# Kernel tuning notes

Hardware: AMD Instinct MI355X
Metric: run time of the kernel (lower is better)

## Reference

```python
import math
import jax, jax.numpy as jnp
from jax import lax
import numpy as np

N = 512          # transform size; frame size = 2N
B = 16           # batch
T = 2048         # number of frames; signal length = N*T
PI = math.pi


def _make_mdct_filter(n: int, normalize: bool = True) -> jnp.ndarray:
    # filter[k, 0, t] = cos(pi/N * (t + 0.5 + N/2) * (k + 0.5)) / sqrt(N)
    k = jnp.arange(n, dtype=jnp.float32).reshape(n, 1, 1)
    t = jnp.arange(2 * n, dtype=jnp.float32).reshape(1, 1, 2 * n)
    f = jnp.cos(PI / n * (t + 0.5 + n / 2) * (k + 0.5))
    if normalize:
        f = f / jnp.sqrt(jnp.float32(n))
    return f  # [N, 1, 2N]


def setup_inputs() -> dict:
    key = jax.random.key(0)
    x = jax.random.normal(key, (B, 1, N * T), dtype=jnp.float32)
    mdct_filter = _make_mdct_filter(N, normalize=True)
    return {"x": x, "mdct_filter": mdct_filter}


def reference(x, mdct_filter):
    # Equivalent of F.conv1d(x, filter, stride=N, padding=N)
    n = mdct_filter.shape[0]
    # x: [B, 1, N*T] -> out: [B, N, T+1]
    out = lax.conv_general_dilated(
        x, mdct_filter,
        window_strides=(n,),
        padding=[(n, n)],
        dimension_numbers=("NCH", "OIH", "NCH"),
    )
    return out
```

## Files before the change

kernel.cpp:

```cpp
#include <hip/hip_runtime.h>
#include <hip/hip_bf16.h>
#include <stdint.h>
#include <stddef.h>


constexpr int N_ = 512;
constexpr int T_ = 2048;
constexpr int B_ = 16;
constexpr int LEN = N_ * T_;
constexpr int FRAMES = T_ + 1;
constexpr int COLS = B_ * FRAMES;
constexpr int NT_TILES = 257;
constexpr int COLS_PAD = NT_TILES * 128;
constexpr int KF = 512;
constexpr int BK = 64;

typedef __attribute__((ext_vector_type(8))) _Float16 f16x8;
typedef __attribute__((ext_vector_type(4))) _Float16 f16x4;
typedef __attribute__((ext_vector_type(4))) float f32x4;

#define GLD16(gptr, lptr)                                                     \
  __builtin_amdgcn_global_load_lds(                                           \
      (const __attribute__((address_space(1))) unsigned int*)(gptr),          \
      (__attribute__((address_space(3))) unsigned int*)(lptr), 16, 0, 0)

__global__ void prep_filter(const float* __restrict__ f,
                            _Float16* __restrict__ D) {
  int idx = (blockIdx.x * 256 + threadIdx.x) * 4;
  int k = idx >> 9;
  int j = idx & 511;
  int t = (j < 256) ? j : (j + 256);
  const float4 v = *(const float4*)&f[k * 1024 + t];
  f16x4 h = {(_Float16)v.x, (_Float16)v.y, (_Float16)v.z, (_Float16)v.w};
  *(f16x4*)&D[k * KF + j] = h;
}

__global__ void fold_x(const float* __restrict__ x, _Float16* __restrict__ V) {
  const int blk = (blockIdx.x & 7) * 1028 + (blockIdx.x >> 3);
  const int c = blk * 4 + (threadIdx.x >> 6);
  const int l = threadIdx.x & 63;
  const bool mi = (l < 32);
  const int j0 = mi ? (l * 8) : (256 + (l - 32) * 8);
  const float sgn = mi ? -1.0f : 1.0f;
  float4 a0 = {0.f, 0.f, 0.f, 0.f}, a1 = {0.f, 0.f, 0.f, 0.f};
  float4 r0 = {0.f, 0.f, 0.f, 0.f}, r1 = {0.f, 0.f, 0.f, 0.f};
  if (c < COLS) {
    int b = (int)((unsigned)c / (unsigned)FRAMES);
    int o = c - b * FRAMES;
    const int lo = b * LEN;
    const int g = lo + o * N_ - N_;
    const int fb = g + (mi ? j0 : (j0 + 256));
    const int rb = g + (mi ? (504 - j0) : (1272 - j0));
    if ((unsigned)(fb - lo) <= (unsigned)(LEN - 8)) {
      a0 = *(const float4*)(x + fb);
      a1 = *(const float4*)(x + fb + 4);
    }
    if ((unsigned)(rb - lo) <= (unsigned)(LEN - 8)) {
      r0 = *(const float4*)(x + rb);
      r1 = *(const float4*)(x + rb + 4);
    }
  }
  f16x8 h;
  h[0] = (_Float16)__builtin_fmaf(sgn, r1.w, a0.x);
  h[1] = (_Float16)__builtin_fmaf(sgn, r1.z, a0.y);
  h[2] = (_Float16)__builtin_fmaf(sgn, r1.y, a0.z);
  h[3] = (_Float16)__builtin_fmaf(sgn, r1.x, a0.w);
  h[4] = (_Float16)__builtin_fmaf(sgn, r0.w, a1.x);
  h[5] = (_Float16)__builtin_fmaf(sgn, r0.z, a1.y);
  h[6] = (_Float16)__builtin_fmaf(sgn, r0.y, a1.z);
  h[7] = (_Float16)__builtin_fmaf(sgn, r0.x, a1.w);
  if (c < COLS_PAD) *(f16x8*)&V[(size_t)c * KF + j0] = h;
}

__global__ __launch_bounds__(256, 4) void gemm_fold(
    const _Float16* __restrict__ D, const _Float16* __restrict__ V,
    float* __restrict__ out) {
  __shared__ __align__(16) _Float16 As[128 * BK];
  __shared__ __align__(16) _Float16 Bs[128 * BK];

  const int id = blockIdx.x;
  const int xcd = id & 7;
  const int sb = id >> 3;
  const int nt = (sb >> 2) * 8 + xcd;
  if (nt >= NT_TILES) return;
  const int m0 = (sb & 3) * 128;
  const int n0 = nt * 128;

  const int tid = threadIdx.x;
  const int wid = tid >> 6;
  const int lane = tid & 63;
  const int quad = lane >> 4;
  const int l16 = lane & 15;
  const int mw = (wid >> 1) * 64;
  const int nw = (wid & 1) * 64;

  f32x4 acc[4][4];
#pragma unroll
  for (int i = 0; i < 4; ++i)
#pragma unroll
    for (int j = 0; j < 4; ++j) acc[i][j] = (f32x4){0.f, 0.f, 0.f, 0.f};

  for (int kt = 0; kt < KF / BK; ++kt) {
    const int kb = kt * BK;
    __syncthreads();
#pragma unroll
    for (int it = 0; it < 4; ++it) {
      const int S = it * 256 + tid;
      const int r = S >> 3;
      const int c = (S & 7) ^ (r & 7);
      const int goff = kb + c * 8;
      GLD16(D + (size_t)(m0 + r) * KF + goff, &As[S * 8]);
      GLD16(V + (size_t)(n0 + r) * KF + goff, &Bs[S * 8]);
    }
    __syncthreads();

#pragma unroll
    for (int ko = 0; ko < 2; ++ko) {
      f16x8 af[4], bf[4];
#pragma unroll
      for (int i = 0; i < 4; ++i) {
        int ra = mw + i * 16 + l16;
        int rb = nw + i * 16 + l16;
        int ca = ko * 4 + quad;
        af[i] = *(const f16x8*)&As[(ra * 8 + (ca ^ (ra & 7))) * 8];
        bf[i] = *(const f16x8*)&Bs[(rb * 8 + (ca ^ (rb & 7))) * 8];
      }
#pragma unroll
      for (int i = 0; i < 4; ++i)
#pragma unroll
        for (int j = 0; j < 4; ++j)
          acc[i][j] = __builtin_amdgcn_mfma_f32_16x16x32_f16(af[i], bf[j], acc[i][j], 0, 0, 0);
    }
  }

#pragma unroll
  for (int i = 0; i < 4; ++i) {
#pragma unroll
    for (int j = 0; j < 4; ++j) {
      int col = n0 + nw + j * 16 + l16;
      if (col < COLS) {
        int b = col / FRAMES;
        int o = col - b * FRAMES;
        int rowb = m0 + mw + i * 16 + quad * 4;
        float* op = out + (size_t)b * N_ * FRAMES + (size_t)rowb * FRAMES + o;
#pragma unroll
        for (int r = 0; r < 4; ++r) op[(size_t)r * FRAMES] = acc[i][j][r];
      }
    }
  }
}

__global__ void naive_conv(const float* __restrict__ x, const float* __restrict__ f,
                           float* __restrict__ out) {
  int col = blockIdx.x;
  int k = threadIdx.x;
  __shared__ float win[1024];
  int b = col / FRAMES;
  int o = col - b * FRAMES;
  const float* xb = x + (size_t)b * LEN;
  int g = o * N_ - N_;
  for (int t = threadIdx.x; t < 1024; t += 512) {
    int i = g + t;
    win[t] = (i >= 0 && i < LEN) ? xb[i] : 0.0f;
  }
  __syncthreads();
  float s = 0.0f;
  const float* fk = f + (size_t)k * 1024;
  for (int t = 0; t < 1024; ++t) s += win[t] * fk[t];
  out[(size_t)b * N_ * FRAMES + (size_t)k * FRAMES + o] = s;
}

extern "C" void kernel_launch(void* const* d_in, const int* in_sizes, int n_in,
                              void* d_out, int out_size, void* d_ws, size_t ws_size,
                              hipStream_t stream) {
  const float* x = (const float*)d_in[0];
  const float* f = (const float*)d_in[1];
  float* out = (float*)d_out;

  const size_t elems_D = (size_t)512 * 512;
  const size_t elems_V = (size_t)COLS_PAD * KF;
  const size_t need = (elems_D + elems_V) * sizeof(_Float16);

  if (ws_size < need) {
    naive_conv<<<COLS, 512, 0, stream>>>(x, f, out);
    return;
  }

  _Float16* D = (_Float16*)d_ws;
  _Float16* V = D + elems_D;

  prep_filter<<<256, 256, 0, stream>>>(f, D);
  fold_x<<<COLS_PAD / 4, 256, 0, stream>>>(x, V);
  gemm_fold<<<1056, 256, 0, stream>>>(D, V, out);
}
```

Before: 147.8 us.

## Double-buffer LDS tiles in the folded MDCT GEMM to overlap loads with MFMA

Splits the GEMM's shared-memory tiles into two ping-pong buffers. The loop is unrolled so the next K-slice's global-to-LDS loads are issued before computing on the current slice. This halves the barriers per K-step and hides load latency behind MFMA work. In exchange, LDS use per block doubles and the occupancy hint drops from 4 to 2 blocks per CU. Correctness also relies on the barrier waiting for the outstanding LDS DMA loads, which is only waited on explicitly for the first stage.

```diff
diff --git a/kernel.cpp b/kernel.cpp
--- a/kernel.cpp
+++ b/kernel.cpp
@@ -14,6 +14,7 @@
 constexpr int COLS_PAD = NT_TILES * 128;
 constexpr int KF = 512;
 constexpr int BK = 64;
+constexpr int TILE_H = 128 * BK;
 
 typedef __attribute__((ext_vector_type(8))) _Float16 f16x8;
 typedef __attribute__((ext_vector_type(4))) _Float16 f16x4;
@@ -72,11 +73,13 @@
   if (c < COLS_PAD) *(f16x8*)&V[(size_t)c * KF + j0] = h;
 }
 
-__global__ __launch_bounds__(256, 4) void gemm_fold(
+__global__ __launch_bounds__(256, 2) void gemm_fold(
     const _Float16* __restrict__ D, const _Float16* __restrict__ V,
     float* __restrict__ out) {
-  __shared__ __align__(16) _Float16 As[128 * BK];
-  __shared__ __align__(16) _Float16 Bs[128 * BK];
+  __shared__ __align__(16) _Float16 As0[TILE_H];
+  __shared__ __align__(16) _Float16 Bs0[TILE_H];
+  __shared__ __align__(16) _Float16 As1[TILE_H];
+  __shared__ __align__(16) _Float16 Bs1[TILE_H];
 
   const int id = blockIdx.x;
   const int xcd = id & 7;
@@ -100,38 +103,62 @@
 #pragma unroll
     for (int j = 0; j < 4; ++j) acc[i][j] = (f32x4){0.f, 0.f, 0.f, 0.f};
 
-  for (int kt = 0; kt < KF / BK; ++kt) {
-    const int kb = kt * BK;
+#define STAGE(AS, BS, KT)                                                     \
+  do {                                                                        \
+    const int kb_ = (KT) * BK;                                                \
+    _Pragma("unroll")                                                         \
+    for (int it = 0; it < 4; ++it) {                                          \
+      const int S_ = it * 256 + tid;      \
+      const int r_ = S_ >> 3;                                   \
+      const int c_ = (S_ & 7) ^ (r_ & 7);          \
+      const int g_ = kb_ + c_ * 8;                                            \
+      GLD16(D + (size_t)(m0 + r_) * KF + g_, &(AS)[S_ * 8]);                  \
+      GLD16(V + (size_t)(n0 + r_) * KF + g_, &(BS)[S_ * 8]);                  \
+    }                                                                         \
+  } while (0)
+
+#define COMPUTE(AS, BS)                                                       \
+  do {                                                                        \
+    _Pragma("unroll")                                                         \
+    for (int ko = 0; ko < 2; ++ko) {                                          \
+      f16x8 af[4], bf[4];                                                     \
+      _Pragma("unroll")                                                       \
+      for (int i = 0; i < 4; ++i) {                                           \
+        int ra_ = mw + i * 16 + l16;                                          \
+        int rb_ = nw + i * 16 + l16;                                          \
+        int ca_ = ko * 4 + quad;                                              \
+        af[i] = *(const f16x8*)&(AS)[(ra_ * 8 + (ca_ ^ (ra_ & 7))) * 8];      \
+        bf[i] = *(const f16x8*)&(BS)[(rb_ * 8 + (ca_ ^ (rb_ & 7))) * 8];      \
+      }                                                                       \
+      _Pragma("unroll")                                                       \
+      for (int i = 0; i < 4; ++i)                                             \
+        _Pragma("unroll")                                                     \
+        for (int j = 0; j < 4; ++j)                                           \
+          acc[i][j] = __builtin_amdgcn_mfma_f32_16x16x32_f16(af[i], bf[j],    \
+                                                             acc[i][j],      \
+                                                             0, 0, 0);        \
+    }                                                                         \
+  } while (0)
+
+  STAGE(As0, Bs0, 0);
+  asm volatile("s_waitcnt vmcnt(0)");
+  __syncthreads();
+
+#pragma unroll
+  for (int kp = 0; kp < 4; ++kp) {
+    STAGE(As1, Bs1, kp * 2 + 1);
+    COMPUTE(As0, Bs0);
     __syncthreads();
-#pragma unroll
-    for (int it = 0; it < 4; ++it) {
-      const int S = it * 256 + tid;
-      const int r = S >> 3;
-      const int c = (S & 7) ^ (r & 7);
-      const int goff = kb + c * 8;
-      GLD16(D + (size_t)(m0 + r) * KF + goff, &As[S * 8]);
-      GLD16(V + (size_t)(n0 + r) * KF + goff, &Bs[S * 8]);
-    }
-    __syncthreads();
-
-#pragma unroll
-    for (int ko = 0; ko < 2; ++ko) {
-      f16x8 af[4], bf[4];
-#pragma unroll
-      for (int i = 0; i < 4; ++i) {
-        int ra = mw + i * 16 + l16;
-        int rb = nw + i * 16 + l16;
-        int ca = ko * 4 + quad;
-        af[i] = *(const f16x8*)&As[(ra * 8 + (ca ^ (ra & 7))) * 8];
-        bf[i] = *(const f16x8*)&Bs[(rb * 8 + (ca ^ (rb & 7))) * 8];
-      }
-#pragma unroll
-      for (int i = 0; i < 4; ++i)
-#pragma unroll
-        for (int j = 0; j < 4; ++j)
-          acc[i][j] = __builtin_amdgcn_mfma_f32_16x16x32_f16(af[i], bf[j], acc[i][j], 0, 0, 0);
-    }
-  }
+    if (kp < 3) {
+      STAGE(As0, Bs0, kp * 2 + 2);
+      COMPUTE(As1, Bs1);
+      __syncthreads();
+    } else {
+      COMPUTE(As1, Bs1);
+    }
+  }
+#undef STAGE
+#undef COMPUTE
 
 #pragma unroll
   for (int i = 0; i < 4; ++i) {
```

Measured after the change: 146.6 us. Within noise of the previous version (-0.8%).
